# Performance work log

Hardware: AMD Instinct MI355X
Metric: run time of the kernel (lower is better)

Reference implementation:

```python
import jax, jax.numpy as jnp
import numpy as np

T_MAX = 4
TOP_K = 4
TEMP = 1.0
THRESH = 0.99
EPS = 1e-6


def _to_c(x):
    return x[..., 0] + 1j * x[..., 1]


def _from_c(z):
    return jnp.stack([z.real, z.imag], axis=-1)


def _forward(psi, bank_keys, bank_vals, u_halt, W_halt, b_halt, head_mix, out_scale):
    B, T, d, _ = psi.shape
    H = bank_keys.shape[0]
    psi_flat = psi.reshape(B * T, d, 2)
    BT = psi_flat.shape[0]
    psi_h = jnp.broadcast_to(psi_flat[:, None], (BT, H, d, 2))
    cum = jnp.zeros((BT, H), psi.dtype)
    halted = jnp.zeros((BT, H), bool)
    cost = jnp.zeros((BT, H), psi.dtype)
    acc = jnp.zeros((BT, H, d, 2), psi.dtype)
    # normalized halt target vectors u (OrthoHalt)
    uc = _to_c(u_halt)  # [H,d] complex
    un = uc / jnp.sqrt(jnp.sum(uc.real**2 + uc.imag**2, -1, keepdims=True) + EPS)
    hidx = jnp.arange(H)
    for it in range(T_MAX):  # fixed small reasoning depth (structural loop)
        is_last = it == T_MAX - 1
        psi_pool = psi_h.mean(axis=1)                       # [BT,d,2]
        feat = psi_pool.reshape(BT, 2 * d)
        # effect-bank probe + top-k gather
        scores = jnp.einsum('bf,hnf->bhn', feat, bank_keys) / TEMP
        w = jax.nn.softmax(scores, axis=-1)                 # [BT,H,N]
        topw, topi = jax.lax.top_k(w, TOP_K)                # [BT,H,K]
        vecs = bank_vals[hidx[None, :, None], topi]         # [BT,H,K,d,2]
        U = _to_c(vecs) * topw[..., None].astype(jnp.complex64)  # weighted basis
        # rank-K Sasaki projection: Pi_F psi = A (A^H A)^{-1} A^H psi, A = U^T
        psic = _to_c(psi_h)                                 # [BT,H,d]
        m = jnp.einsum('bhkd,bhd->bhk', jnp.conj(U), psic)
        G = jnp.einsum('bhkd,bhjd->bhkj', jnp.conj(U), U)
        G = G + EPS * jnp.eye(TOP_K, dtype=G.dtype)
        coeff = jnp.linalg.solve(G, m[..., None])[..., 0]
        proj = jnp.einsum('bhkd,bhk->bhd', U, coeff)
        psi_next = _from_c(proj)
        # renormalize_psi
        sq = (psi_next[..., 0] ** 2 + psi_next[..., 1] ** 2).sum(-1, keepdims=True)
        psi_next = psi_next / jnp.sqrt(jnp.maximum(sq, 1e-6))[..., None]
        # OrthoHalt on pooled next state -> (alpha, beta, gamma) -> 3 logits
        pool_next = _to_c(psi_next.mean(axis=1))            # [BT,d]
        c = jnp.einsum('hd,bd->bh', jnp.conj(un), pool_next)
        ns = jnp.sum(pool_next.real**2 + pool_next.imag**2, -1)[:, None] + EPS
        alpha = (c.real**2 + c.imag**2) / ns
        beta = 1.0 - alpha
        gamma = c.real**2 / ns
        abg = jnp.stack([alpha, beta, gamma], -1)           # [BT,H,3]
        logits = jnp.einsum('bhi,hij->bhj', abg, W_halt) + b_halt
        probs = jax.nn.softmax(logits, -1)
        p_halt = probs[..., 0] + probs[..., 1]              # yes + no mass
        # ACT ponder update
        would = cum + p_halt
        halts_now = jnp.logical_or(would >= THRESH, is_last)
        active = jnp.logical_not(halted)
        weight = jnp.where(active, jnp.where(halts_now, 1.0 - cum, p_halt), 0.0)
        cost = cost + jnp.where(active, p_halt, 0.0)
        cum = jnp.where(jnp.logical_and(active, jnp.logical_not(halts_now)), would, cum)
        halted = jnp.logical_or(halted, jnp.logical_and(active, halts_now))
        acc = acc + weight[..., None, None] * psi_next
        psi_h = psi_next
    head_w = jax.nn.softmax(head_mix)[None, :, None, None]
    merged = (acc * head_w).sum(axis=1)                     # [BT,d,2]
    residual = merged - psi_flat
    psi_out = (psi_flat + out_scale * residual).reshape(B, T, d, 2)
    return psi_out, cost.mean()


def setup_inputs() -> dict:
    key = jax.random.key(0)
    ks = jax.random.split(key, 6)
    B, T, d, H, N = 2, 2048, 512, 4, 2048
    psi = jax.random.normal(ks[0], (B, T, d, 2), jnp.float32)
    psi = psi / jnp.sqrt(jnp.maximum((psi**2).sum((-1, -2), keepdims=True), 1e-6))
    bank_keys = 0.05 * jax.random.normal(ks[1], (H, N, 2 * d), jnp.float32)
    bank_vals = jax.random.normal(ks[2], (H, N, d, 2), jnp.float32)
    u_halt = jax.random.normal(ks[3], (H, d, 2), jnp.float32)
    W_halt = jax.random.normal(ks[4], (H, 3, 3), jnp.float32)
    b_halt = jnp.zeros((H, 3), jnp.float32)
    head_mix = jnp.zeros((H,), jnp.float32)
    out_scale = jnp.asarray(0.1, jnp.float32)
    return dict(psi=psi, bank_keys=bank_keys, bank_vals=bank_vals, u_halt=u_halt,
                W_halt=W_halt, b_halt=b_halt, head_mix=head_mix, out_scale=out_scale)


def reference(psi, bank_keys, bank_vals, u_halt, W_halt, b_halt, head_mix, out_scale):
    return _forward(psi, bank_keys, bank_vals, u_halt, W_halt, b_halt, head_mix, out_scale)
```

## Files before the change

kernel.cpp:

```cpp
#include <hip/hip_runtime.h>
#include <math.h>

#define HH 4
#define DD 512
#define FF 1024
#define NN 2048
#define KK 4
#define TMAXI 4
#define THRESHV 0.99f
#define EPSV 1e-6f

typedef unsigned short ushort_t;
typedef __attribute__((ext_vector_type(8))) __bf16 bf16x8;
typedef __attribute__((ext_vector_type(8))) _Float16 half8;
typedef __attribute__((ext_vector_type(4))) float f32x4;
typedef __attribute__((ext_vector_type(4))) unsigned short us4;

__device__ __forceinline__ unsigned short f2bf(float x) {
    unsigned int u = __float_as_uint(x);
    unsigned int r = (u + 0x7FFF + ((u >> 16) & 1)) >> 16;
    return (unsigned short)r;
}

__device__ __forceinline__ float fast_rcp(float x) { return __builtin_amdgcn_rcpf(x); }

typedef __attribute__((address_space(3))) unsigned int lds_u32;
typedef __attribute__((address_space(1))) const unsigned int glb_u32;
__device__ __forceinline__ void gl_lds16(const void* g, void* s) {
    __builtin_amdgcn_global_load_lds((glb_u32*)g, (lds_u32*)s, 16, 0, 0);
}

__global__ void k_unorm(const float* __restrict__ u_halt, float* __restrict__ norm_inv) {
    __shared__ float red[256];
    int tid = threadIdx.x;
    for (int h = 0; h < HH; ++h) {
        float s = 0.f;
        for (int i = tid; i < FF; i += 256) { float v = u_halt[h * FF + i]; s += v * v; }
        red[tid] = s; __syncthreads();
        for (int off = 128; off > 0; off >>= 1) {
            if (tid < off) red[tid] += red[tid + off];
            __syncthreads();
        }
        if (tid == 0) norm_inv[h] = 1.0f / sqrtf(red[0] + EPSV);
        __syncthreads();
    }
}

__global__ void k_cvt_bf(const float* __restrict__ in, ushort_t* __restrict__ out, int total) {
    int i = blockIdx.x * 256 + threadIdx.x;
    if (i >= total) return;
    out[i] = f2bf(in[i]);
}

#define BM 128
#define BN 128
#define BKE 64
__global__ __launch_bounds__(256) void k_gemm_mfma(const ushort_t* __restrict__ A,
                                                   const ushort_t* __restrict__ B,
                                                   ushort_t* __restrict__ C) {
    __shared__ __align__(16) ushort_t As[BM * BKE];
    __shared__ __align__(16) ushort_t Bs[BN * BKE];
    int tid = threadIdx.x;
    int lane = tid & 63, w = tid >> 6;
    int row0 = blockIdx.y * BM, col0 = blockIdx.x * BN;

    int srow = lane >> 3;
    int schunk = (lane & 7) ^ srow;
    const ushort_t* gA = A + (size_t)(row0 + w * 32 + srow) * FF + schunk * 8;
    const ushort_t* gB = B + (size_t)(col0 + w * 32 + srow) * FF + schunk * 8;
    ushort_t* sA = As + (w * 32) * BKE;
    ushort_t* sB = Bs + (w * 32) * BKE;

    int fr = lane & 15;
    int q  = lane >> 4;
    int wr0 = (w >> 1) * 64, wc0 = (w & 1) * 64;

    f32x4 acc[4][4] = {};

    for (int kb = 0; kb < FF; kb += BKE) {
        #pragma unroll
        for (int i = 0; i < 4; i++) {
            gl_lds16(gA + kb + (size_t)(8 * i) * FF, sA + (8 * i) * BKE);
            gl_lds16(gB + kb + (size_t)(8 * i) * FF, sB + (8 * i) * BKE);
        }
        __syncthreads();
        bf16x8 af[2][4], bfv[2][4];
        #pragma unroll
        for (int hf = 0; hf < 2; hf++) {
            int ck = ((4 * hf + q) ^ (fr & 7)) * 8;
            #pragma unroll
            for (int i = 0; i < 4; i++) {
                af[hf][i]  = *(const bf16x8*)&As[(wr0 + 16 * i + fr) * BKE + ck];
                bfv[hf][i] = *(const bf16x8*)&Bs[(wc0 + 16 * i + fr) * BKE + ck];
            }
        }
        #pragma unroll
        for (int hf = 0; hf < 2; hf++)
            #pragma unroll
            for (int i = 0; i < 4; i++)
                #pragma unroll
                for (int j = 0; j < 4; j++)
                    acc[i][j] = __builtin_amdgcn_mfma_f32_16x16x32_bf16(af[hf][i], bfv[hf][j], acc[i][j], 0, 0, 0);
        __syncthreads();
    }

    int crow = (lane >> 4) * 4;
    int ccol = lane & 15;
    #pragma unroll
    for (int i = 0; i < 4; i++)
        #pragma unroll
        for (int r = 0; r < 4; r++) {
            ushort_t* Cr = C + (size_t)(row0 + wr0 + 16 * i + crow + r) * (HH * NN) + col0 + wc0 + ccol;
            #pragma unroll
            for (int j = 0; j < 4; j++) {
                _Float16 hv = (_Float16)acc[i][j][r];
                Cr[16 * j] = *(ushort_t*)&hv;
            }
        }
}

__global__ __launch_bounds__(256) void k_softtop(const ushort_t* __restrict__ Sc,
                                                 float* __restrict__ topw, int* __restrict__ topi,
                                                 int row0) {
    int tid = threadIdx.x;
    int w = tid >> 6, lane = tid & 63;
    int g = blockIdx.x * 4 + w;
    int r = g >> 2;
    int h = g & 3;
    const ushort_t* S = Sc + (size_t)r * (HH * NN) + h * NN + lane * 8;
    float f0[8], f1[8], f2[8], f3[8];
    {
        half8 h0 = *(const half8*)(S);
        half8 h1 = *(const half8*)(S + 512);
        half8 h2 = *(const half8*)(S + 1024);
        half8 h3 = *(const half8*)(S + 1536);
        #pragma unroll
        for (int e = 0; e < 8; e++) {
            f0[e] = (float)h0[e]; f1[e] = (float)h1[e];
            f2[e] = (float)h2[e]; f3[e] = (float)h3[e];
        }
    }

    float bm = f0[0];
    #pragma unroll
    for (int e = 0; e < 8; e++) {
        bm = fmaxf(bm, fmaxf(fmaxf(f0[e], f1[e]), fmaxf(f2[e], f3[e])));
    }
    #pragma unroll
    for (int m = 1; m < 64; m <<= 1) bm = fmaxf(bm, __shfl_xor(bm, m, 64));

    float se = 0.f;
    #pragma unroll
    for (int e = 0; e < 8; e++)
        se += __expf(f0[e] - bm) + __expf(f1[e] - bm) + __expf(f2[e] - bm) + __expf(f3[e] - bm);
    #pragma unroll
    for (int m = 1; m < 64; m <<= 1) se += __shfl_xor(se, m, 64);
    float Zinv = fast_rcp(se);

    int gbh = (row0 + r) * HH + h;
    int base = lane * 8;
    #pragma unroll
    for (int k = 0; k < KK; k++) {
        float bv = -INFINITY; int bi = NN;
        #pragma unroll
        for (int e = 0; e < 8; e++) {
            if (f0[e] > bv) { bv = f0[e]; bi = base + e; }
        }
        #pragma unroll
        for (int e = 0; e < 8; e++) {
            if (f1[e] > bv) { bv = f1[e]; bi = 512 + base + e; }
        }
        #pragma unroll
        for (int e = 0; e < 8; e++) {
            if (f2[e] > bv) { bv = f2[e]; bi = 1024 + base + e; }
        }
        #pragma unroll
        for (int e = 0; e < 8; e++) {
            if (f3[e] > bv) { bv = f3[e]; bi = 1536 + base + e; }
        }
        #pragma unroll
        for (int m = 1; m < 64; m <<= 1) {
            float ov = __shfl_xor(bv, m, 64);
            int   oi = __shfl_xor(bi, m, 64);
            if (ov > bv || (ov == bv && oi < bi)) { bv = ov; bi = oi; }
        }
        if (lane == 0) {
            topw[gbh * KK + k] = __expf(bv - bm) * Zinv;
            topi[gbh * KK + k] = bi;
        }
        if (k < KK - 1) {
            #pragma unroll
            for (int e = 0; e < 8; e++) {
                if (base + e == bi)        f0[e] = -INFINITY;
                if (512 + base + e == bi)  f1[e] = -INFINITY;
                if (1024 + base + e == bi) f2[e] = -INFINITY;
                if (1536 + base + e == bi) f3[e] = -INFINITY;
            }
        }
    }
}

__global__ __launch_bounds__(256) void k_fused(const float* __restrict__ psi,
                                               float* __restrict__ psi_h,
                                               const float* __restrict__ bank_vals,
                                               const float* __restrict__ topw,
                                               const int* __restrict__ topi,
                                               const float* __restrict__ u_halt,
                                               const float* __restrict__ norm_inv,
                                               const float* __restrict__ W_halt,
                                               const float* __restrict__ b_halt,
                                               const float* __restrict__ head_mix,
                                               float* __restrict__ merged,
                                               ushort_t* __restrict__ feat,
                                               float* __restrict__ cum,
                                               float* __restrict__ cost,
                                               int* __restrict__ halted,
                                               int first, int is_last) {
    __shared__ float Pn[HH][FF];
    __shared__ float xw[4][9];
    int b = blockIdx.x;
    int tid = threadIdx.x;
    int w = tid >> 6, lane = tid & 63;
    int bh = b * HH + w;

    float wk[KK]; int ix[KK];
    #pragma unroll
    for (int k = 0; k < KK; k++) { wk[k] = topw[bh * KK + k]; ix[k] = topi[bh * KK + k]; }

    const float* Pr = first ? (psi + (size_t)b * FF) : (psi_h + (size_t)bh * FF);
    float4 p4[4], v4[KK][4];
    #pragma unroll
    for (int c = 0; c < 4; c++) p4[c] = *(const float4*)(Pr + lane * 16 + 4 * c);
    #pragma unroll
    for (int k = 0; k < KK; k++) {
        const float* Vp = bank_vals + ((size_t)(w * NN) + ix[k]) * FF + lane * 16;
        #pragma unroll
        for (int c = 0; c < 4; c++) v4[k][c] = *(const float4*)(Vp + 4 * c);
    }

    float part[24];
    #pragma unroll
    for (int t = 0; t < 24; t++) part[t] = 0.f;
    #pragma unroll
    for (int c = 0; c < 4; c++) {
        #pragma unroll
        for (int e = 0; e < 2; e++) {
            float prr = e ? p4[c].z : p4[c].x;
            float pii = e ? p4[c].w : p4[c].y;
            float vr[KK], vi[KK];
            #pragma unroll
            for (int k = 0; k < KK; k++) {
                vr[k] = e ? v4[k][c].z : v4[k][c].x;
                vi[k] = e ? v4[k][c].w : v4[k][c].y;
            }
            #pragma unroll
            for (int k = 0; k < KK; k++) {
                part[2 * k]     += vr[k] * prr + vi[k] * pii;
                part[2 * k + 1] += vr[k] * pii - vi[k] * prr;
                part[8 + k]     += vr[k] * vr[k] + vi[k] * vi[k];
            }
            int t = 12;
            #pragma unroll
            for (int k = 0; k < KK; k++)
                #pragma unroll
                for (int j = k + 1; j < KK; j++) {
                    part[t]     += vr[k] * vr[j] + vi[k] * vi[j];
                    part[t + 1] += vr[k] * vi[j] - vi[k] * vr[j];
                    t += 2;
                }
        }
    }
    #pragma unroll
    for (int m = 1; m < 64; m <<= 1)
        #pragma unroll
        for (int t = 0; t < 24; t++) part[t] += __shfl_xor(part[t], m, 64);

    float mr[KK], mi[KK], Gr[KK][KK], Gi[KK][KK];
    #pragma unroll
    for (int k = 0; k < KK; k++) {
        mr[k] = part[2 * k] * wk[k];
        mi[k] = part[2 * k + 1] * wk[k];
        Gr[k][k] = part[8 + k] * wk[k] * wk[k] + EPSV;
        Gi[k][k] = 0.f;
    }
    {
        int t = 12;
        #pragma unroll
        for (int k = 0; k < KK; k++)
            #pragma unroll
            for (int j = k + 1; j < KK; j++) {
                float s = wk[k] * wk[j];
                Gr[k][j] = part[t] * s;  Gi[k][j] = part[t + 1] * s;
                Gr[j][k] = Gr[k][j];     Gi[j][k] = -Gi[k][j];
                t += 2;
            }
    }

    float Lr[KK][KK], Li[KK][KK];
    #pragma unroll
    for (int j = 0; j < KK; j++) {
        float s = Gr[j][j];
        #pragma unroll
        for (int p = 0; p < KK; p++) if (p < j) s -= Lr[j][p] * Lr[j][p] + Li[j][p] * Li[j][p];
        float ljj = sqrtf(fmaxf(s, 1e-30f));
        Lr[j][j] = ljj; Li[j][j] = 0.f;
        float inv = 1.0f / ljj;
        #pragma unroll
        for (int k = 0; k < KK; k++) {
            if (k > j) {
                float ar = Gr[k][j], ai = Gi[k][j];
                #pragma unroll
                for (int p = 0; p < KK; p++) if (p < j) {
                    ar -= Lr[k][p] * Lr[j][p] + Li[k][p] * Li[j][p];
                    ai -= Li[k][p] * Lr[j][p] - Lr[k][p] * Li[j][p];
                }
                Lr[k][j] = ar * inv; Li[k][j] = ai * inv;
            }
        }
    }
    float yr[KK], yi[KK];
    #pragma unroll
    for (int j = 0; j < KK; j++) {
        float ar = mr[j], ai = mi[j];
        #pragma unroll
        for (int p = 0; p < KK; p++) if (p < j) {
            ar -= Lr[j][p] * yr[p] - Li[j][p] * yi[p];
            ai -= Lr[j][p] * yi[p] + Li[j][p] * yr[p];
        }
        float inv = 1.0f / Lr[j][j];
        yr[j] = ar * inv; yi[j] = ai * inv;
    }
    float xr[KK], xi2[KK];
    #pragma unroll
    for (int j = KK - 1; j >= 0; j--) {
        float ar = yr[j], ai = yi[j];
        #pragma unroll
        for (int p = 0; p < KK; p++) if (p > j) {
            ar -= Lr[p][j] * xr[p] + Li[p][j] * xi2[p];
            ai -= Lr[p][j] * xi2[p] - Li[p][j] * xr[p];
        }
        float inv = 1.0f / Lr[j][j];
        xr[j] = ar * inv; xi2[j] = ai * inv;
    }
    float cxr[KK], cxi[KK];
    #pragma unroll
    for (int k = 0; k < KK; k++) { cxr[k] = xr[k] * wk[k]; cxi[k] = xi2[k] * wk[k]; }

    float4 pj[4];
    float sqp = 0.f;
    #pragma unroll
    for (int c = 0; c < 4; c++) {
        float ar0 = 0.f, ai0 = 0.f, ar1 = 0.f, ai1 = 0.f;
        #pragma unroll
        for (int k = 0; k < KK; k++) {
            ar0 += v4[k][c].x * cxr[k] - v4[k][c].y * cxi[k];
            ai0 += v4[k][c].x * cxi[k] + v4[k][c].y * cxr[k];
            ar1 += v4[k][c].z * cxr[k] - v4[k][c].w * cxi[k];
            ai1 += v4[k][c].z * cxi[k] + v4[k][c].w * cxr[k];
        }
        pj[c].x = ar0; pj[c].y = ai0; pj[c].z = ar1; pj[c].w = ai1;
        sqp += ar0 * ar0 + ai0 * ai0 + ar1 * ar1 + ai1 * ai1;
    }
    #pragma unroll
    for (int m = 1; m < 64; m <<= 1) sqp += __shfl_xor(sqp, m, 64);
    float rn = 1.0f / sqrtf(fmaxf(sqp, 1e-6f));

    float* Pdst = psi_h + (size_t)bh * FF + lane * 16;
    #pragma unroll
    for (int c = 0; c < 4; c++) {
        float4 o; o.x = pj[c].x * rn; o.y = pj[c].y * rn; o.z = pj[c].z * rn; o.w = pj[c].w * rn;
        if (!is_last) *(float4*)(Pdst + 4 * c) = o;
        *(float4*)&Pn[w][lane * 16 + 4 * c] = o;
    }
    __syncthreads();

    int t4 = tid * 4;
    float4 a0 = *(const float4*)&Pn[0][t4];
    float4 a1 = *(const float4*)&Pn[1][t4];
    float4 a2 = *(const float4*)&Pn[2][t4];
    float4 a3 = *(const float4*)&Pn[3][t4];
    float4 pool;
    pool.x = 0.25f * (a0.x + a1.x + a2.x + a3.x);
    pool.y = 0.25f * (a0.y + a1.y + a2.y + a3.y);
    pool.z = 0.25f * (a0.z + a1.z + a2.z + a3.z);
    pool.w = 0.25f * (a0.w + a1.w + a2.w + a3.w);

    float pt[9];
    #pragma unroll
    for (int h = 0; h < HH; h++) {
        float4 u = *(const float4*)&u_halt[h * FF + t4];
        pt[2 * h]     = u.x * pool.x + u.y * pool.y + u.z * pool.z + u.w * pool.w;
        pt[2 * h + 1] = u.x * pool.y - u.y * pool.x + u.z * pool.w - u.w * pool.z;
    }
    pt[8] = pool.x * pool.x + pool.y * pool.y + pool.z * pool.z + pool.w * pool.w;
    #pragma unroll
    for (int m = 1; m < 64; m <<= 1)
        #pragma unroll
        for (int t = 0; t < 9; t++) pt[t] += __shfl_xor(pt[t], m, 64);
    if (lane == 0) {
        #pragma unroll
        for (int t = 0; t < 9; t++) xw[w][t] = pt[t];
    }
    __syncthreads();
    float red[9];
    #pragma unroll
    for (int t = 0; t < 9; t++) red[t] = xw[0][t] + xw[1][t] + xw[2][t] + xw[3][t];
    float ns = red[8] + EPSV;

    float hm0 = head_mix[0], hm1 = head_mix[1], hm2 = head_mix[2], hm3 = head_mix[3];
    float hmx = fmaxf(fmaxf(hm0, hm1), fmaxf(hm2, hm3));
    float he[4] = {expf(hm0 - hmx), expf(hm1 - hmx), expf(hm2 - hmx), expf(hm3 - hmx)};
    float hsum = he[0] + he[1] + he[2] + he[3];

    float wgt[4], addc[4], newcum[4]; int newhl[4];
    int idxb = b * HH;
    #pragma unroll
    for (int h = 0; h < HH; h++) {
        float cr = red[2 * h] * norm_inv[h], ci = red[2 * h + 1] * norm_inv[h];
        float alpha = (cr * cr + ci * ci) / ns;
        float beta = 1.0f - alpha;
        float gamma = cr * cr / ns;
        float lg[3];
        #pragma unroll
        for (int j = 0; j < 3; j++)
            lg[j] = alpha * W_halt[(h * 3 + 0) * 3 + j] + beta * W_halt[(h * 3 + 1) * 3 + j] +
                    gamma * W_halt[(h * 3 + 2) * 3 + j] + b_halt[h * 3 + j];
        float mx = fmaxf(lg[0], fmaxf(lg[1], lg[2]));
        float e0 = expf(lg[0] - mx), e1 = expf(lg[1] - mx), e2 = expf(lg[2] - mx);
        float p_halt = (e0 + e1) / (e0 + e1 + e2);
        float cm = cum[idxb + h];
        int hl = halted[idxb + h];
        float would = cm + p_halt;
        int halts_now = (would >= THRESHV) || is_last;
        int active = hl ? 0 : 1;
        wgt[h]  = active ? (halts_now ? (1.0f - cm) : p_halt) : 0.0f;
        addc[h] = active ? p_halt : 0.0f;
        newcum[h] = (active && !halts_now) ? would : cm;
        newhl[h]  = hl || (active && halts_now);
    }
    __syncthreads();
    if (tid < HH) {
        cost[idxb + tid] += addc[tid];
        cum[idxb + tid] = newcum[tid];
        halted[idxb + tid] = newhl[tid];
    }
    float hwv[4];
    #pragma unroll
    for (int h = 0; h < HH; h++) hwv[h] = (he[h] / hsum) * wgt[h];

    size_t mo = (size_t)b * FF + t4;
    float4 m4 = *(const float4*)&merged[mo];
    m4.x += hwv[0] * a0.x + hwv[1] * a1.x + hwv[2] * a2.x + hwv[3] * a3.x;
    m4.y += hwv[0] * a0.y + hwv[1] * a1.y + hwv[2] * a2.y + hwv[3] * a3.y;
    m4.z += hwv[0] * a0.z + hwv[1] * a1.z + hwv[2] * a2.z + hwv[3] * a3.z;
    m4.w += hwv[0] * a0.w + hwv[1] * a1.w + hwv[2] * a2.w + hwv[3] * a3.w;
    *(float4*)&merged[mo] = m4;

    if (!is_last) {
        us4 fb;
        fb.x = f2bf(pool.x); fb.y = f2bf(pool.y); fb.z = f2bf(pool.z); fb.w = f2bf(pool.w);
        *(us4*)&feat[mo] = fb;
    }
}

__global__ void k_out(const float* __restrict__ psi, const float* __restrict__ merged,
                      const float* __restrict__ out_scale, float* __restrict__ out, int total) {
    int i = blockIdx.x * 256 + threadIdx.x;
    if (i >= total) return;
    float p = psi[i];
    out[i] = p + out_scale[0] * (merged[i] - p);
}

__global__ void k_costmean(const float* __restrict__ cost, float* __restrict__ out, int n) {
    __shared__ float red[256];
    int tid = threadIdx.x;
    float s = 0.f;
    for (int i = tid; i < n; i += 256) s += cost[i];
    red[tid] = s; __syncthreads();
    for (int off = 128; off > 0; off >>= 1) {
        if (tid < off) red[tid] += red[tid + off];
        __syncthreads();
    }
    if (tid == 0) out[0] = red[0] / (float)n;
}

extern "C" void kernel_launch(void* const* d_in, const int* in_sizes, int n_in,
                              void* d_out, int out_size, void* d_ws, size_t ws_size,
                              hipStream_t stream) {
    const float* psi       = (const float*)d_in[0];
    const float* bank_keys = (const float*)d_in[1];
    const float* bank_vals = (const float*)d_in[2];
    const float* u_halt    = (const float*)d_in[3];
    const float* W_halt    = (const float*)d_in[4];
    const float* b_halt    = (const float*)d_in[5];
    const float* head_mix  = (const float*)d_in[6];
    const float* out_scale = (const float*)d_in[7];
    float* out = (float*)d_out;

    const int BT = in_sizes[0] / FF;

    float* ws = (float*)d_ws;
    size_t off = 0;
    float* psi_h  = ws + off; off += (size_t)BT * HH * FF;
    float* merged = ws + off; off += (size_t)BT * FF;
    float* cum    = ws + off; off += (size_t)BT * HH;
    float* costv  = ws + off; off += (size_t)BT * HH;
    int*   halted = (int*)(ws + off); off += (size_t)BT * HH;
    float* topw   = ws + off; off += (size_t)BT * HH * KK;
    int*   topi   = (int*)(ws + off); off += (size_t)BT * HH * KK;
    float* norminv = ws + off; off += 16;
    ushort_t* feat_bf = (ushort_t*)(ws + off); off += (size_t)BT * FF / 2;
    ushort_t* keys_bf = (ushort_t*)(ws + off); off += (size_t)HH * NN * FF / 2;
    ushort_t* scores = (ushort_t*)(ws + off);
    size_t fixed = off;

    size_t ws_floats = ws_size / 4;
    int RC = BT;
    while (RC > 128 && fixed + (size_t)RC * HH * NN / 2 > ws_floats) RC >>= 1;
    int nchunks = BT / RC;

    hipMemsetAsync(merged, 0, ((size_t)BT * FF + 3 * (size_t)BT * HH) * sizeof(float), stream);
    k_unorm<<<1, 256, 0, stream>>>(u_halt, norminv);
    int tot_keys = HH * NN * FF;
    k_cvt_bf<<<(tot_keys + 255) / 256, 256, 0, stream>>>(bank_keys, keys_bf, tot_keys);
    int tot_bf = BT * FF;
    k_cvt_bf<<<(tot_bf + 255) / 256, 256, 0, stream>>>(psi, feat_bf, tot_bf);

    for (int it = 0; it < TMAXI; ++it) {
        for (int c = 0; c < nchunks; ++c) {
            k_gemm_mfma<<<dim3((HH * NN) / BN, RC / BM), 256, 0, stream>>>(
                feat_bf + (size_t)c * RC * FF, keys_bf, scores);
            k_softtop<<<dim3((RC * HH) / 4), 256, 0, stream>>>(scores, topw, topi, c * RC);
        }
        k_fused<<<BT, 256, 0, stream>>>(psi, psi_h, bank_vals, topw, topi, u_halt, norminv,
                                        W_halt, b_halt, head_mix, merged, feat_bf,
                                        cum, costv, halted,
                                        (it == 0) ? 1 : 0, (it == TMAXI - 1) ? 1 : 0);
    }
    k_out<<<(tot_bf + 255) / 256, 256, 0, stream>>>(psi, merged, out_scale, out, tot_bf);
    k_costmean<<<1, 256, 0, stream>>>(costv, out + tot_bf, BT * HH);
}
```

Measured before the change: 1.056 ms.

## Store per-head state in fp16, fuse output epilogue, vectorize bf16 conversion

```diff
diff --git a/kernel.cpp b/kernel.cpp
--- a/kernel.cpp
+++ b/kernel.cpp
@@ -46,10 +46,13 @@
     }
 }
 
-__global__ void k_cvt_bf(const float* __restrict__ in, ushort_t* __restrict__ out, int total) {
+__global__ void k_cvt_bf4(const float* __restrict__ in, ushort_t* __restrict__ out, int total4) {
     int i = blockIdx.x * 256 + threadIdx.x;
-    if (i >= total) return;
-    out[i] = f2bf(in[i]);
+    if (i >= total4) return;
+    float4 v = ((const float4*)in)[i];
+    us4 o;
+    o.x = f2bf(v.x); o.y = f2bf(v.y); o.z = f2bf(v.z); o.w = f2bf(v.w);
+    ((us4*)out)[i] = o;
 }
 
 #define BM 128
@@ -201,7 +204,7 @@
 }
 
 __global__ __launch_bounds__(256) void k_fused(const float* __restrict__ psi,
-                                               float* __restrict__ psi_h,
+                                               ushort_t* __restrict__ psi_h,
                                                const float* __restrict__ bank_vals,
                                                const float* __restrict__ topw,
                                                const int* __restrict__ topi,
@@ -215,6 +218,8 @@
                                                float* __restrict__ cum,
                                                float* __restrict__ cost,
                                                int* __restrict__ halted,
+                                               const float* __restrict__ out_scale,
+                                               float* __restrict__ outbuf,
                                                int first, int is_last) {
     __shared__ float Pn[HH][FF];
     __shared__ float xw[4][9];
@@ -227,10 +232,20 @@
     #pragma unroll
     for (int k = 0; k < KK; k++) { wk[k] = topw[bh * KK + k]; ix[k] = topi[bh * KK + k]; }
 
-    const float* Pr = first ? (psi + (size_t)b * FF) : (psi_h + (size_t)bh * FF);
     float4 p4[4], v4[KK][4];
-    #pragma unroll
-    for (int c = 0; c < 4; c++) p4[c] = *(const float4*)(Pr + lane * 16 + 4 * c);
+    if (first) {
+        const float* Pr = psi + (size_t)b * FF + lane * 16;
+        #pragma unroll
+        for (int c = 0; c < 4; c++) p4[c] = *(const float4*)(Pr + 4 * c);
+    } else {
+        const ushort_t* Ph = psi_h + (size_t)bh * FF + lane * 16;
+        half8 ha = *(const half8*)(Ph);
+        half8 hb = *(const half8*)(Ph + 8);
+        p4[0].x = (float)ha[0]; p4[0].y = (float)ha[1]; p4[0].z = (float)ha[2]; p4[0].w = (float)ha[3];
+        p4[1].x = (float)ha[4]; p4[1].y = (float)ha[5]; p4[1].z = (float)ha[6]; p4[1].w = (float)ha[7];
+        p4[2].x = (float)hb[0]; p4[2].y = (float)hb[1]; p4[2].z = (float)hb[2]; p4[2].w = (float)hb[3];
+        p4[3].x = (float)hb[4]; p4[3].y = (float)hb[5]; p4[3].z = (float)hb[6]; p4[3].w = (float)hb[7];
+    }
     #pragma unroll
     for (int k = 0; k < KK; k++) {
         const float* Vp = bank_vals + ((size_t)(w * NN) + ix[k]) * FF + lane * 16;
@@ -365,12 +380,24 @@
     for (int m = 1; m < 64; m <<= 1) sqp += __shfl_xor(sqp, m, 64);
     float rn = 1.0f / sqrtf(fmaxf(sqp, 1e-6f));
 
-    float* Pdst = psi_h + (size_t)bh * FF + lane * 16;
-    #pragma unroll
-    for (int c = 0; c < 4; c++) {
-        float4 o; o.x = pj[c].x * rn; o.y = pj[c].y * rn; o.z = pj[c].z * rn; o.w = pj[c].w * rn;
-        if (!is_last) *(float4*)(Pdst + 4 * c) = o;
-        *(float4*)&Pn[w][lane * 16 + 4 * c] = o;
+    float4 o0, o1, o2, o3;
+    o0.x = pj[0].x * rn; o0.y = pj[0].y * rn; o0.z = pj[0].z * rn; o0.w = pj[0].w * rn;
+    o1.x = pj[1].x * rn; o1.y = pj[1].y * rn; o1.z = pj[1].z * rn; o1.w = pj[1].w * rn;
+    o2.x = pj[2].x * rn; o2.y = pj[2].y * rn; o2.z = pj[2].z * rn; o2.w = pj[2].w * rn;
+    o3.x = pj[3].x * rn; o3.y = pj[3].y * rn; o3.z = pj[3].z * rn; o3.w = pj[3].w * rn;
+    *(float4*)&Pn[w][lane * 16 + 0]  = o0;
+    *(float4*)&Pn[w][lane * 16 + 4]  = o1;
+    *(float4*)&Pn[w][lane * 16 + 8]  = o2;
+    *(float4*)&Pn[w][lane * 16 + 12] = o3;
+    if (!is_last) {
+        half8 wa, wb;
+        wa[0] = (_Float16)o0.x; wa[1] = (_Float16)o0.y; wa[2] = (_Float16)o0.z; wa[3] = (_Float16)o0.w;
+        wa[4] = (_Float16)o1.x; wa[5] = (_Float16)o1.y; wa[6] = (_Float16)o1.z; wa[7] = (_Float16)o1.w;
+        wb[0] = (_Float16)o2.x; wb[1] = (_Float16)o2.y; wb[2] = (_Float16)o2.z; wb[3] = (_Float16)o2.w;
+        wb[4] = (_Float16)o3.x; wb[5] = (_Float16)o3.y; wb[6] = (_Float16)o3.z; wb[7] = (_Float16)o3.w;
+        ushort_t* Pd = psi_h + (size_t)bh * FF + lane * 16;
+        *(half8*)(Pd)     = wa;
+        *(half8*)(Pd + 8) = wb;
     }
     __syncthreads();
 
@@ -454,21 +481,21 @@
     m4.y += hwv[0] * a0.y + hwv[1] * a1.y + hwv[2] * a2.y + hwv[3] * a3.y;
     m4.z += hwv[0] * a0.z + hwv[1] * a1.z + hwv[2] * a2.z + hwv[3] * a3.z;
     m4.w += hwv[0] * a0.w + hwv[1] * a1.w + hwv[2] * a2.w + hwv[3] * a3.w;
-    *(float4*)&merged[mo] = m4;
-
-    if (!is_last) {
+    if (is_last) {
+        float4 pp = *(const float4*)&psi[mo];
+        float os = out_scale[0];
+        float4 ov;
+        ov.x = pp.x + os * (m4.x - pp.x);
+        ov.y = pp.y + os * (m4.y - pp.y);
+        ov.z = pp.z + os * (m4.z - pp.z);
+        ov.w = pp.w + os * (m4.w - pp.w);
+        *(float4*)&outbuf[mo] = ov;
+    } else {
+        *(float4*)&merged[mo] = m4;
         us4 fb;
         fb.x = f2bf(pool.x); fb.y = f2bf(pool.y); fb.z = f2bf(pool.z); fb.w = f2bf(pool.w);
         *(us4*)&feat[mo] = fb;
     }
-}
-
-__global__ void k_out(const float* __restrict__ psi, const float* __restrict__ merged,
-                      const float* __restrict__ out_scale, float* __restrict__ out, int total) {
-    int i = blockIdx.x * 256 + threadIdx.x;
-    if (i >= total) return;
-    float p = psi[i];
-    out[i] = p + out_scale[0] * (merged[i] - p);
 }
 
 __global__ void k_costmean(const float* __restrict__ cost, float* __restrict__ out, int n) {
@@ -501,7 +528,7 @@
 
     float* ws = (float*)d_ws;
     size_t off = 0;
-    float* psi_h  = ws + off; off += (size_t)BT * HH * FF;
+    ushort_t* psi_h = (ushort_t*)(ws + off); off += (size_t)BT * HH * FF / 2;
     float* merged = ws + off; off += (size_t)BT * FF;
     float* cum    = ws + off; off += (size_t)BT * HH;
     float* costv  = ws + off; off += (size_t)BT * HH;
@@ -512,31 +539,21 @@
     ushort_t* feat_bf = (ushort_t*)(ws + off); off += (size_t)BT * FF / 2;
     ushort_t* keys_bf = (ushort_t*)(ws + off); off += (size_t)HH * NN * FF / 2;
     ushort_t* scores = (ushort_t*)(ws + off);
-    size_t fixed = off;
-
-    size_t ws_floats = ws_size / 4;
-    int RC = BT;
-    while (RC > 128 && fixed + (size_t)RC * HH * NN / 2 > ws_floats) RC >>= 1;
-    int nchunks = BT / RC;
 
     hipMemsetAsync(merged, 0, ((size_t)BT * FF + 3 * (size_t)BT * HH) * sizeof(float), stream);
     k_unorm<<<1, 256, 0, stream>>>(u_halt, norminv);
     int tot_keys = HH * NN * FF;
-    k_cvt_bf<<<(tot_keys + 255) / 256, 256, 0, stream>>>(bank_keys, keys_bf, tot_keys);
+    k_cvt_bf4<<<(tot_keys / 4 + 255) / 256, 256, 0, stream>>>(bank_keys, keys_bf, tot_keys / 4);
     int tot_bf = BT * FF;
-    k_cvt_bf<<<(tot_bf + 255) / 256, 256, 0, stream>>>(psi, feat_bf, tot_bf);
+    k_cvt_bf4<<<(tot_bf / 4 + 255) / 256, 256, 0, stream>>>(psi, feat_bf, tot_bf / 4);
 
     for (int it = 0; it < TMAXI; ++it) {
-        for (int c = 0; c < nchunks; ++c) {
-            k_gemm_mfma<<<dim3((HH * NN) / BN, RC / BM), 256, 0, stream>>>(
-                feat_bf + (size_t)c * RC * FF, keys_bf, scores);
-            k_softtop<<<dim3((RC * HH) / 4), 256, 0, stream>>>(scores, topw, topi, c * RC);
-        }
+        k_gemm_mfma<<<dim3((HH * NN) / BN, BT / BM), 256, 0, stream>>>(feat_bf, keys_bf, scores);
+        k_softtop<<<dim3((BT * HH) / 4), 256, 0, stream>>>(scores, topw, topi, 0);
         k_fused<<<BT, 256, 0, stream>>>(psi, psi_h, bank_vals, topw, topi, u_halt, norminv,
                                         W_halt, b_halt, head_mix, merged, feat_bf,
-                                        cum, costv, halted,
+                                        cum, costv, halted, out_scale, out,
                                         (it == 0) ? 1 : 0, (it == TMAXI - 1) ? 1 : 0);
     }
-    k_out<<<(tot_bf + 255) / 256, 256, 0, stream>>>(psi, merged, out_scale, out, tot_bf);
     k_costmean<<<1, 256, 0, stream>>>(costv, out + tot_bf, BT * HH);
 }
```

Result: slower. 1.311 ms (+24.2%).
